# Kernel tuning notes

Hardware: AMD Instinct MI355X
Metric: run time of the kernel (lower is better)

Reference implementation:

```python
import jax, jax.numpy as jnp
import numpy as np

DIM, NH, HD = 1536, 12, 128
C = HD // 2            # 64 complex (half) dims per head
BANDS = (C - 2 * (C // 3), C // 3, C // 3)   # (22, 21, 21) for T/H/W
EPS = 1e-6
F, Hg, Wg = 6, 20, 32
S = F * Hg * Wg
MAX_LEN = 1024


def _rope_tables(max_len=MAX_LEN):
    # Wan-style 1D rope params per band, concatenated along channel dim -> [max_len, 64]
    pos = np.arange(max_len, dtype=np.float64)
    cos_l, sin_l = [], []
    for bd in BANDS:
        inv = 1.0 / (10000.0 ** (np.arange(bd, dtype=np.float64) / bd))
        ang = np.outer(pos, inv)
        cos_l.append(np.cos(ang))
        sin_l.append(np.sin(ang))
    return (np.concatenate(cos_l, 1).astype(np.float32),
            np.concatenate(sin_l, 1).astype(np.float32))


def setup_inputs() -> dict:
    key = jax.random.key(0)
    ks = jax.random.split(key, 8)
    std = 0.02
    fc, fs = _rope_tables()
    return {
        "x": jax.random.normal(ks[0], (1, S, DIM), jnp.float32),
        "Wq": jax.random.normal(ks[1], (DIM, DIM), jnp.float32) * std,
        "bq": jnp.zeros((DIM,), jnp.float32),
        "Wk": jax.random.normal(ks[2], (DIM, DIM), jnp.float32) * std,
        "bk": jnp.zeros((DIM,), jnp.float32),
        "Wv": jax.random.normal(ks[3], (DIM, DIM), jnp.float32) * std,
        "bv": jnp.zeros((DIM,), jnp.float32),
        "Wo": jax.random.normal(ks[4], (DIM, DIM), jnp.float32) * std,
        "bo": jnp.zeros((DIM,), jnp.float32),
        "gq": jnp.ones((DIM,), jnp.float32),
        "gk": jnp.ones((DIM,), jnp.float32),
        "freqs_cos": jnp.asarray(fc),
        "freqs_sin": jnp.asarray(fs),
        "f": F, "h": Hg, "w": Wg,
    }


def _rmsnorm(t, g):
    t = t.astype(jnp.float32)
    return t * jax.lax.rsqrt(jnp.mean(t * t, axis=-1, keepdims=True) + EPS) * g


def _grid_freqs(tab, f, h, w):
    # tab: [max_len, 64] -> [f*h*w, 64] via T/H/W band broadcast (mirrors torch expand+cat)
    o1, o2 = BANDS[0], BANDS[0] + BANDS[1]
    t = jnp.broadcast_to(tab[:f, None, None, :o1], (f, h, w, BANDS[0]))
    hh = jnp.broadcast_to(tab[None, :h, None, o1:o2], (f, h, w, BANDS[1]))
    ww = jnp.broadcast_to(tab[None, None, :w, o2:C], (f, h, w, BANDS[2]))
    return jnp.concatenate([t, hh, ww], axis=-1).reshape(f * h * w, 1, C)


def _rope_apply(t, fc, fs):
    # t: [B, S, n, d]; complex mul (a+ib)*(cos+isin) on pairs of channels
    B, Sl, n, d = t.shape
    tr = t.astype(jnp.float32).reshape(B, Sl, n, C, 2)
    a, b = tr[..., 0], tr[..., 1]
    fc = fc[None]  # [1, S, 1, C]
    fs = fs[None]
    out_r = a * fc - b * fs
    out_i = a * fs + b * fc
    return jnp.stack([out_r, out_i], axis=-1).reshape(B, Sl, n, d)


def reference(x, Wq, bq, Wk, bk, Wv, bv, Wo, bo, gq, gk, freqs_cos, freqs_sin, f, h, w):
    B, Sl, _ = x.shape
    q = _rmsnorm(x @ Wq.T + bq, gq).reshape(B, Sl, NH, HD)
    k = _rmsnorm(x @ Wk.T + bk, gk).reshape(B, Sl, NH, HD)
    v = (x @ Wv.T + bv).reshape(B, Sl, NH, HD)

    fc = _grid_freqs(freqs_cos, f, h, w)
    fs = _grid_freqs(freqs_sin, f, h, w)
    q = _rope_apply(q, fc, fs)
    k = _rope_apply(k, fc, fs)

    scale = 1.0 / jnp.sqrt(jnp.float32(HD))
    scores = jnp.einsum('bqnd,bknd->bnqk', q, k) * scale
    p = jax.nn.softmax(scores, axis=-1)
    o = jnp.einsum('bnqk,bknd->bqnd', p, v.astype(jnp.float32))
    o = o.reshape(B, Sl, DIM)
    return o @ Wo.T + bo
```

## Files before the change

kernel.cpp:

```cpp
#include <hip/hip_runtime.h>
#include <hip/hip_bf16.h>
#include <cstdint>

#define DIM 1536
#define NHEADS 12
#define HD 128
#define SEQ 3840
#define SCL2F 0.1275365308119098f
#define THRRAW 90.50966799187809f

typedef float f32x4 __attribute__((ext_vector_type(4)));
typedef __bf16 bf16x8 __attribute__((ext_vector_type(8)));
typedef __bf16 bf16x4 __attribute__((ext_vector_type(4)));
typedef __bf16 bf16x2 __attribute__((ext_vector_type(2)));
typedef unsigned int u32;
typedef u32 u32x4 __attribute__((ext_vector_type(4)));

#define GLLD(g, l) __builtin_amdgcn_global_load_lds( \
    (const __attribute__((address_space(1))) void*)(g), \
    (__attribute__((address_space(3))) void*)(l), 16, 0, 0)

__global__ __launch_bounds__(256) void cvt_bf16_5(
    const float* __restrict__ s0, const float* __restrict__ s1, const float* __restrict__ s2,
    const float* __restrict__ s3, const float* __restrict__ s4,
    __bf16* __restrict__ d0, __bf16* __restrict__ d1, __bf16* __restrict__ d2,
    __bf16* __restrict__ d3, __bf16* __restrict__ d4,
    int n4_0, int n4_w) {
    const float* src; __bf16* dst; int n4;
    switch (blockIdx.y) {
        case 0: src = s0; dst = d0; n4 = n4_0; break;
        case 1: src = s1; dst = d1; n4 = n4_w; break;
        case 2: src = s2; dst = d2; n4 = n4_w; break;
        case 3: src = s3; dst = d3; n4 = n4_w; break;
        default: src = s4; dst = d4; n4 = n4_w; break;
    }
    int i = blockIdx.x * 256 + threadIdx.x;
    if (i < n4) {
        f32x4 v = ((const f32x4*)src)[i];
        bf16x4 o;
        o[0] = (__bf16)v[0]; o[1] = (__bf16)v[1];
        o[2] = (__bf16)v[2]; o[3] = (__bf16)v[3];
        ((bf16x4*)dst)[i] = o;
    }
}

template <int OUTF32>
__global__ __launch_bounds__(256, 2) void gemm256(
    const __bf16* __restrict__ A,
    const __bf16* __restrict__ B0, const __bf16* __restrict__ B1, const __bf16* __restrict__ B2,
    const float* __restrict__ bias0, const float* __restrict__ bias1, const float* __restrict__ bias2,
    void* __restrict__ C0v, void* __restrict__ C1v, void* __restrict__ C2v,
    int N, int K) {
    const int orig = blockIdx.x;
    const int nwg = gridDim.x;
    const int qq_ = nwg >> 3, rr_ = nwg & 7;
    const int xcd = orig & 7, off = orig >> 3;
    const int wgid = (xcd < rr_ ? xcd * (qq_ + 1) : rr_ * (qq_ + 1) + (xcd - rr_) * qq_) + off;
    const int z = wgid / 180;
    const int rem = wgid - z * 180;
    const int by = rem / 12;
    const int bx = rem - by * 12;

    const __bf16* B = B0; const float* bias = bias0; void* Cv = C0v;
    if (z == 1) { B = B1; bias = bias1; Cv = C1v; }
    else if (z == 2) { B = B2; bias = bias2; Cv = C2v; }

    __shared__ __bf16 sA[3][256 * 32];
    __shared__ __bf16 sB[3][128 * 32];

    const int t = threadIdx.x;
    const int wid = t >> 6, lane = t & 63;
    const int lr = lane & 15, lg = lane >> 4;
    const int wr = (wid >> 1) * 128, wc = (wid & 1) * 64;

    const __bf16* pa = A + ((long long)by * 256 + (t >> 2)) * K + (t & 3) * 8;
    const __bf16* pb = B + ((long long)bx * 128 + (t >> 2)) * K + (t & 3) * 8;
    const int ldsbase = wid * 512;

    auto stage = [&](int kk, int bufi) {
#pragma unroll
        for (int r = 0; r < 4; r++)
            GLLD(pa + (long long)(r * 64) * K + kk, &sA[bufi][r * 2048 + ldsbase]);
#pragma unroll
        for (int r = 0; r < 2; r++)
            GLLD(pb + (long long)(r * 64) * K + kk, &sB[bufi][r * 2048 + ldsbase]);
    };

    f32x4 acc[8][4] = {};
    const int NT = K / 32;

    stage(0, 0);
    stage(32, 1);
    asm volatile("s_waitcnt vmcnt(6)" ::: "memory");
    __builtin_amdgcn_s_barrier();
    __builtin_amdgcn_sched_barrier(0);

    int c0 = 0, c2 = 2;
#pragma unroll 1
    for (int i = 0; i < NT; i++) {
        const __bf16* sAc = &sA[0][0] + c0 * (256 * 32);
        const __bf16* sBc = &sB[0][0] + c0 * (128 * 32);
        bf16x8 af[8], bfr[4];
#pragma unroll
        for (int mI = 0; mI < 8; mI++)
            af[mI] = *(const bf16x8*)(sAc + (wr + mI * 16 + lr) * 32 + lg * 8);
#pragma unroll
        for (int nI = 0; nI < 4; nI++)
            bfr[nI] = *(const bf16x8*)(sBc + (wc + nI * 16 + lr) * 32 + lg * 8);
        if (i + 2 < NT) stage((i + 2) * 32, c2);

        __builtin_amdgcn_s_setprio(1);
#pragma unroll
        for (int mI = 0; mI < 8; mI++) {
            acc[mI][0] = __builtin_amdgcn_mfma_f32_16x16x32_bf16(af[mI], bfr[0], acc[mI][0], 0, 0, 0);
            acc[mI][1] = __builtin_amdgcn_mfma_f32_16x16x32_bf16(af[mI], bfr[1], acc[mI][1], 0, 0, 0);
        }
        __builtin_amdgcn_s_setprio(0);
        __builtin_amdgcn_s_barrier();
        __builtin_amdgcn_s_setprio(1);
#pragma unroll
        for (int mI = 0; mI < 8; mI++) {
            acc[mI][2] = __builtin_amdgcn_mfma_f32_16x16x32_bf16(af[mI], bfr[2], acc[mI][2], 0, 0, 0);
            acc[mI][3] = __builtin_amdgcn_mfma_f32_16x16x32_bf16(af[mI], bfr[3], acc[mI][3], 0, 0, 0);
        }
        __builtin_amdgcn_s_setprio(0);

        if (i + 2 < NT) asm volatile("s_waitcnt vmcnt(6)" ::: "memory");
        else            asm volatile("s_waitcnt vmcnt(0)" ::: "memory");
        __builtin_amdgcn_s_barrier();
        __builtin_amdgcn_sched_barrier(0);
        c0 = (c0 == 2) ? 0 : c0 + 1;
        c2 = (c2 == 2) ? 0 : c2 + 1;
    }

    const int cb = bx * 128 + wc;
    const int rb_ = by * 256 + wr;
#pragma unroll
    for (int nI = 0; nI < 4; nI++) {
        int col = cb + nI * 16 + lr;
        float bv = bias[col];
#pragma unroll
        for (int mI = 0; mI < 8; mI++) {
            int row0 = rb_ + mI * 16 + lg * 4;
#pragma unroll
            for (int r = 0; r < 4; r++) {
                float v = acc[mI][nI][r] + bv;
                if (OUTF32) ((float*)Cv)[(long long)(row0 + r) * N + col] = v;
                else ((__bf16*)Cv)[(long long)(row0 + r) * N + col] = (__bf16)v;
            }
        }
    }
}

__global__ __launch_bounds__(256) void norm_rope2(
    const __bf16* __restrict__ qpre, const __bf16* __restrict__ kpre,
    const float* __restrict__ gq, const float* __restrict__ gk,
    const float* __restrict__ fcos, const float* __restrict__ fsin,
    __bf16* __restrict__ Qb, __bf16* __restrict__ Kb) {
    const __bf16* pre = blockIdx.y ? kpre : qpre;
    const float* gvec = blockIdx.y ? gk : gq;
    __bf16* out = blockIdx.y ? Kb : Qb;
    const int s = blockIdx.x;
    const int t = threadIdx.x;
    float a[3], b[3];
    float ss = 0.f;
#pragma unroll
    for (int j = 0; j < 3; j++) {
        int p = t + 256 * j;
        bf16x2 v = *(const bf16x2*)(pre + (size_t)s * DIM + 2 * p);
        a[j] = (float)v[0]; b[j] = (float)v[1];
        ss += a[j] * a[j] + b[j] * b[j];
    }
    for (int off = 32; off; off >>= 1) ss += __shfl_down(ss, off);
    __shared__ float red[4];
    if ((t & 63) == 0) red[t >> 6] = ss;
    __syncthreads();
    float mean = (red[0] + red[1] + red[2] + red[3]) * (1.f / DIM);
    float rms = rsqrtf(mean + 1e-6f);
    const int fi = s / 640, hi2 = (s % 640) >> 5, wi = s & 31;
#pragma unroll
    for (int j = 0; j < 3; j++) {
        int p = t + 256 * j;
        int c = p & 63;
        int pos = (c < 22) ? fi : ((c < 43) ? hi2 : wi);
        float fc = fcos[pos * 64 + c];
        float fs = fsin[pos * 64 + c];
        float av = a[j] * rms * gvec[2 * p];
        float bv = b[j] * rms * gvec[2 * p + 1];
        float orr = av * fc - bv * fs;
        float oi = av * fs + bv * fc;
        int hh = p >> 6;
        bf16x2 o; o[0] = (__bf16)orr; o[1] = (__bf16)oi;
        *(bf16x2*)(out + ((size_t)hh * SEQ + s) * HD + 2 * c) = o;
    }
}

__global__ __launch_bounds__(256) void transpose_bf16(
    const __bf16* __restrict__ in, __bf16* __restrict__ out) {
    __shared__ __bf16 tile[64][68];
    const int t = threadIdx.x;
    const int sb = blockIdx.x * 64, cb = blockIdx.y * 64;
    const int tx = t & 15, ty = t >> 4;
#pragma unroll
    for (int i = 0; i < 4; i++) {
        int r = ty + i * 16;
        bf16x4 v = *(const bf16x4*)(in + (size_t)(sb + r) * DIM + cb + tx * 4);
        *(bf16x4*)&tile[r][tx * 4] = v;
    }
    __syncthreads();
    int s0 = sb + tx * 4;
    int j = (s0 >> 2) & 7;
    int u = (j < 4) ? (j << 1) : ((j << 1) - 7);
    int sp = (s0 & ~31) + (u << 2);
#pragma unroll
    for (int i = 0; i < 4; i++) {
        int c = ty + i * 16;
        bf16x4 v;
        v[0] = tile[tx * 4 + 0][c]; v[1] = tile[tx * 4 + 1][c];
        v[2] = tile[tx * 4 + 2][c]; v[3] = tile[tx * 4 + 3][c];
        *(bf16x4*)(out + (size_t)(cb + c) * SEQ + sp) = v;
    }
}

__global__ __launch_bounds__(256, 3) void attn_split(
    const __bf16* __restrict__ Q, const __bf16* __restrict__ Kk,
    const __bf16* __restrict__ Vp,
    float* __restrict__ pacc,
    float2* __restrict__ pml) {
    __shared__ __bf16 Ks[2][32 * 128];
    __shared__ __bf16 Vs[2][128 * 32];
    const int bid = blockIdx.x;
    const int task = (bid & 7) * 90 + (bid >> 3);
    const int half = task & 1;
    const int hq = task >> 1;
    const int h = hq / 30;
    const int qb = hq % 30;
    const int t = threadIdx.x;
    const int wv = t >> 6;
    const int lane = t & 63;
    const int lq = lane & 15, g = lane >> 4;
    const int q0 = qb * 128 + wv * 32;
    const int kvbase = half * (SEQ / 2);
    const __bf16* Qh = Q + (size_t)h * SEQ * HD;
    const __bf16* Kh = Kk + (size_t)h * SEQ * HD;
    const __bf16* Vh = Vp + (size_t)h * HD * SEQ;

    bf16x8 qf[2][4];
#pragma unroll
    for (int qg = 0; qg < 2; qg++)
#pragma unroll
        for (int c = 0; c < 4; c++)
            qf[qg][c] = *(const bf16x8*)(Qh + (size_t)(q0 + qg * 16 + lq) * HD + c * 32 + g * 8);

    f32x4 acc[8][2] = {};
    float m[2] = {-1e30f, -1e30f};
    float lp[2] = {0.f, 0.f};

    const int krow0 = wv * 4 + (lane >> 4);
    const int kcb = ((lane & 15) * 16) ^ ((krow0 & 7) << 4);
    const __bf16* kp = Kh + (size_t)(kvbase + krow0) * HD + (kcb >> 1);
    const __bf16* vp = Vh + (size_t)(wv * 16 + (lane >> 2)) * SEQ + kvbase + (lane & 3) * 8;
    auto stage = [&](int i, int b) {
        const __bf16* kpi = kp + (size_t)i * 32 * HD;
        const __bf16* vpi = vp + i * 32;
        GLLD(kpi,           &Ks[b][wv * 512]);
        GLLD(kpi + 16 * HD, &Ks[b][(wv + 4) * 512]);
        GLLD(vpi,            &Vs[b][wv * 512]);
        GLLD(vpi + 64 * SEQ, &Vs[b][(wv + 4) * 512]);
    };

    stage(0, 0);
    int buf = 0;
    const int kswz = (lq & 7) << 3;
#pragma unroll 1
    for (int i = 0; i < 60; i++) {
        __syncthreads();
        if (i + 1 < 60) stage(i + 1, buf ^ 1);
        const __bf16* Kb_ = &Ks[buf][0];
        const __bf16* Vb_ = &Vs[buf][0];

        f32x4 sc[2][2] = {};
        __builtin_amdgcn_s_setprio(1);
#pragma unroll
        for (int c = 0; c < 4; c++) {
            int cb = (c * 32 + g * 8) ^ kswz;
            bf16x8 k0 = *(const bf16x8*)(Kb_ + lq * 128 + cb);
            bf16x8 k1 = *(const bf16x8*)(Kb_ + (16 + lq) * 128 + cb);
            sc[0][0] = __builtin_amdgcn_mfma_f32_16x16x32_bf16(k0, qf[0][c], sc[0][0], 0, 0, 0);
            sc[0][1] = __builtin_amdgcn_mfma_f32_16x16x32_bf16(k0, qf[1][c], sc[0][1], 0, 0, 0);
            sc[1][0] = __builtin_amdgcn_mfma_f32_16x16x32_bf16(k1, qf[0][c], sc[1][0], 0, 0, 0);
            sc[1][1] = __builtin_amdgcn_mfma_f32_16x16x32_bf16(k1, qf[1][c], sc[1][1], 0, 0, 0);
        }
        __builtin_amdgcn_s_setprio(0);

        bf16x8 vf[8];
#pragma unroll
        for (int dt = 0; dt < 8; dt++)
            vf[dt] = *(const bf16x8*)(Vb_ + (dt * 16 + lq) * 32 + g * 8);

        bf16x8 pa[2];
#pragma unroll
        for (int qg = 0; qg < 2; qg++) {
            float pm = fmaxf(fmaxf(sc[0][qg][0], sc[0][qg][1]), sc[0][qg][2]);
            pm = fmaxf(fmaxf(pm, sc[0][qg][3]), sc[1][qg][0]);
            pm = fmaxf(fmaxf(pm, sc[1][qg][1]), sc[1][qg][2]);
            pm = fmaxf(pm, sc[1][qg][3]);
            if (!__all(pm <= m[qg] + THRRAW)) {
                pm = fmaxf(pm, __shfl_xor(pm, 16));
                pm = fmaxf(pm, __shfl_xor(pm, 32));
                float mn = fmaxf(m[qg], pm);
                float al = __builtin_amdgcn_exp2f(SCL2F * (m[qg] - mn));
                m[qg] = mn; lp[qg] *= al;
#pragma unroll
                for (int dt = 0; dt < 8; dt++)
#pragma unroll
                    for (int r = 0; r < 4; r++) acc[dt][qg][r] *= al;
            }
            float ms = SCL2F * m[qg];
            float p[8], ls = 0.f;
#pragma unroll
            for (int r = 0; r < 4; r++) { p[r] = __builtin_amdgcn_exp2f(SCL2F * sc[0][qg][r] - ms); ls += p[r]; }
#pragma unroll
            for (int r = 0; r < 4; r++) { p[4 + r] = __builtin_amdgcn_exp2f(SCL2F * sc[1][qg][r] - ms); ls += p[4 + r]; }
            lp[qg] += ls;
#pragma unroll
            for (int i2 = 0; i2 < 8; i2++) pa[qg][i2] = (__bf16)p[i2];
        }

        __builtin_amdgcn_s_setprio(1);
#pragma unroll
        for (int dt = 0; dt < 8; dt++) {
            acc[dt][0] = __builtin_amdgcn_mfma_f32_16x16x32_bf16(vf[dt], pa[0], acc[dt][0], 0, 0, 0);
            acc[dt][1] = __builtin_amdgcn_mfma_f32_16x16x32_bf16(vf[dt], pa[1], acc[dt][1], 0, 0, 0);
        }
        __builtin_amdgcn_s_setprio(0);
        buf ^= 1;
    }

#pragma unroll
    for (int qg = 0; qg < 2; qg++) {
        float lps = lp[qg];
        lps += __shfl_xor(lps, 16);
        lps += __shfl_xor(lps, 32);
        const size_t qrow = (size_t)(half * NHEADS + h) * SEQ + q0 + qg * 16 + lq;
        if (g == 0) pml[qrow] = float2{m[qg], lps};
#pragma unroll
        for (int dt = 0; dt < 8; dt++)
            *(f32x4*)(pacc + qrow * HD + dt * 16 + g * 4) = acc[dt][qg];
    }
}

__global__ __launch_bounds__(256) void attn_merge(
    const float* __restrict__ pacc, const float2* __restrict__ pml,
    __bf16* __restrict__ ob) {
    const int t = threadIdx.x;
    const int qq = blockIdx.x * 8 + (t >> 5);
    const int d = (t & 31) * 4;
    float2 a = pml[qq], b = pml[NHEADS * SEQ + qq];
    float M = fmaxf(a.x, b.x);
    float w0 = __builtin_amdgcn_exp2f(SCL2F * (a.x - M));
    float w1 = __builtin_amdgcn_exp2f(SCL2F * (b.x - M));
    float den = 1.f / (a.y * w0 + b.y * w1);
    f32x4 n0 = *(const f32x4*)(pacc + (size_t)qq * HD + d);
    f32x4 n1 = *(const f32x4*)(pacc + ((size_t)NHEADS * SEQ + qq) * HD + d);
    int h = qq / SEQ, s = qq % SEQ;
    bf16x4 o;
#pragma unroll
    for (int r = 0; r < 4; r++) o[r] = (__bf16)((n0[r] * w0 + n1[r] * w1) * den);
    *(bf16x4*)(ob + (size_t)s * DIM + h * HD + d) = o;
}

__global__ __launch_bounds__(256, 4) void attn_single(
    const __bf16* __restrict__ Q, const __bf16* __restrict__ Kk,
    const __bf16* __restrict__ Vp, __bf16* __restrict__ O) {
    __shared__ __bf16 Ks[2][32 * 128];
    __shared__ __bf16 Vs[2][128 * 32];
    const int bid = blockIdx.x;
    const int task = (bid & 7) * 90 + (bid >> 3);
    const int h = task / 60;
    const int qb = task % 60;
    const int t = threadIdx.x;
    const int wv = t >> 6;
    const int lane = t & 63;
    const int lq = lane & 15, g = lane >> 4;
    const int q0 = qb * 64 + wv * 16;
    const __bf16* Qh = Q + (size_t)h * SEQ * HD;
    const __bf16* Kh = Kk + (size_t)h * SEQ * HD;
    const __bf16* Vh = Vp + (size_t)h * HD * SEQ;
    bf16x8 qf[4];
#pragma unroll
    for (int c = 0; c < 4; c++)
        qf[c] = *(const bf16x8*)(Qh + (size_t)(q0 + lq) * HD + c * 32 + g * 8);
    f32x4 acc[8] = {};
    float m = -1e30f, lp = 0.f;
    const int krow_in = lane >> 4;
    const int vrow_in = lane >> 2;
    const int vce = (lane & 3) * 8;
    auto stage = [&](int kv0, int b) {
#pragma unroll
        for (int c = wv; c < 16; c += 4) {
            if (c < 8) {
                int r = c * 4 + krow_in;
                int cb = ((lane & 15) * 16) ^ ((r & 7) << 4);
                GLLD(Kh + (size_t)(kv0 + r) * HD + (cb >> 1), &Ks[b][c * 512]);
            } else {
                int cc = c - 8;
                int rd = cc * 16 + vrow_in;
                GLLD(Vh + (size_t)rd * SEQ + kv0 + vce, &Vs[b][cc * 512]);
            }
        }
    };
    stage(0, 0);
    int buf = 0;
    const int kswz = (lq & 7) << 3;
#pragma unroll 1
    for (int i = 0; i < 120; i++) {
        __syncthreads();
        if (i + 1 < 120) stage((i + 1) * 32, buf ^ 1);
        const __bf16* Kb_ = &Ks[buf][0];
        const __bf16* Vb_ = &Vs[buf][0];
        f32x4 sc0 = {0.f, 0.f, 0.f, 0.f}, sc1 = {0.f, 0.f, 0.f, 0.f};
#pragma unroll
        for (int c = 0; c < 4; c++) {
            int cb = (c * 32 + g * 8) ^ kswz;
            bf16x8 k0 = *(const bf16x8*)(Kb_ + lq * 128 + cb);
            bf16x8 k1 = *(const bf16x8*)(Kb_ + (16 + lq) * 128 + cb);
            sc0 = __builtin_amdgcn_mfma_f32_16x16x32_bf16(k0, qf[c], sc0, 0, 0, 0);
            sc1 = __builtin_amdgcn_mfma_f32_16x16x32_bf16(k1, qf[c], sc1, 0, 0, 0);
        }
        bf16x8 vf[8];
#pragma unroll
        for (int dt = 0; dt < 8; dt++)
            vf[dt] = *(const bf16x8*)(Vb_ + (dt * 16 + lq) * 32 + g * 8);
        float pm = fmaxf(fmaxf(sc0[0], sc0[1]), sc0[2]);
        pm = fmaxf(fmaxf(pm, sc0[3]), sc1[0]);
        pm = fmaxf(fmaxf(pm, sc1[1]), sc1[2]);
        pm = fmaxf(pm, sc1[3]);
        if (!__all(pm <= m + THRRAW)) {
            pm = fmaxf(pm, __shfl_xor(pm, 16));
            pm = fmaxf(pm, __shfl_xor(pm, 32));
            float mn = fmaxf(m, pm);
            float al = __builtin_amdgcn_exp2f(SCL2F * (m - mn));
            m = mn; lp *= al;
#pragma unroll
            for (int dt = 0; dt < 8; dt++)
#pragma unroll
                for (int r = 0; r < 4; r++) acc[dt][r] *= al;
        }
        float ms = SCL2F * m;
        float p[8], ls = 0.f;
#pragma unroll
        for (int r = 0; r < 4; r++) { p[r] = __builtin_amdgcn_exp2f(SCL2F * sc0[r] - ms); ls += p[r]; }
#pragma unroll
        for (int r = 0; r < 4; r++) { p[4 + r] = __builtin_amdgcn_exp2f(SCL2F * sc1[r] - ms); ls += p[4 + r]; }
        lp += ls;
        bf16x8 pa;
#pragma unroll
        for (int i2 = 0; i2 < 8; i2++) pa[i2] = (__bf16)p[i2];
#pragma unroll
        for (int dt = 0; dt < 8; dt++)
            acc[dt] = __builtin_amdgcn_mfma_f32_16x16x32_bf16(vf[dt], pa, acc[dt], 0, 0, 0);
        buf ^= 1;
    }
    float lps = lp;
    lps += __shfl_xor(lps, 16);
    lps += __shfl_xor(lps, 32);
    float inv = 1.f / lps;
#pragma unroll
    for (int dt = 0; dt < 8; dt++) {
        bf16x4 o;
#pragma unroll
        for (int r = 0; r < 4; r++) o[r] = (__bf16)(acc[dt][r] * inv);
        *(bf16x4*)(O + (size_t)(q0 + lq) * DIM + h * HD + dt * 16 + g * 4) = o;
    }
}

extern "C" void kernel_launch(void* const* d_in, const int* in_sizes, int n_in,
                              void* d_out, int out_size, void* d_ws, size_t ws_size,
                              hipStream_t stream) {
    const float* x = (const float*)d_in[0];
    const float* Wq = (const float*)d_in[1];
    const float* bq = (const float*)d_in[2];
    const float* Wk = (const float*)d_in[3];
    const float* bk = (const float*)d_in[4];
    const float* Wv = (const float*)d_in[5];
    const float* bv = (const float*)d_in[6];
    const float* Wo = (const float*)d_in[7];
    const float* bo = (const float*)d_in[8];
    const float* gq = (const float*)d_in[9];
    const float* gk = (const float*)d_in[10];
    const float* fcos = (const float*)d_in[11];
    const float* fsin = (const float*)d_in[12];
    float* out = (float*)d_out;

    char* p = (char*)d_ws;
    const size_t SZ_SD = (size_t)SEQ * DIM * 2;
    const size_t SZ_W = (size_t)DIM * DIM * 2;
    __bf16* xb   = (__bf16*)p;  p += SZ_SD;
    __bf16* Wob  = (__bf16*)p;  p += SZ_W;
    __bf16* Wqb  = (__bf16*)p;  p += SZ_W;
    __bf16* Wkb  = (__bf16*)p;  p += SZ_W;
    __bf16* Wvb  = (__bf16*)p;  p += SZ_W;
    __bf16* qpre = (__bf16*)p;  p += SZ_SD;
    __bf16* kpre = (__bf16*)p;  p += SZ_SD;
    __bf16* vpre = (__bf16*)p;  p += SZ_SD;
    __bf16* Kb   = (__bf16*)p;  p += SZ_SD;
    __bf16* Vtb  = (__bf16*)p;  p += SZ_SD;
    float2* pml  = (float2*)p;  p += sizeof(float2) * 2 * NHEADS * SEQ;
    float* pacc = (float*)Wqb;
    __bf16* Qb = xb;
    const bool split_ok = ws_size >= (size_t)(p - (char*)d_ws);

    const int n4_x = SEQ * DIM / 4;
    const int n4_w = DIM * DIM / 4;
    cvt_bf16_5<<<dim3((n4_x + 255) / 256, 5), 256, 0, stream>>>(
        x, Wq, Wk, Wv, Wo, xb, Wqb, Wkb, Wvb, Wob, n4_x, n4_w);

    gemm256<0><<<dim3(540), 256, 0, stream>>>(
        xb, Wqb, Wkb, Wvb, bq, bk, bv, qpre, kpre, vpre, DIM, DIM);

    norm_rope2<<<dim3(SEQ, 2), 256, 0, stream>>>(qpre, kpre, gq, gk, fcos, fsin, Qb, Kb);
    transpose_bf16<<<dim3(SEQ / 64, DIM / 64), 256, 0, stream>>>(vpre, Vtb);

    if (split_ok) {
        __bf16* ob = Kb;
        attn_split<<<dim3(720), 256, 0, stream>>>(Qb, Kb, Vtb, pacc, pml);
        attn_merge<<<dim3(NHEADS * SEQ / 8), 256, 0, stream>>>(pacc, pml, ob);
        gemm256<1><<<dim3(180), 256, 0, stream>>>(
            ob, Wob, Wob, Wob, bo, bo, bo, out, out, out, DIM, DIM);
    } else {
        __bf16* ob = qpre;
        attn_single<<<dim3(720), 256, 0, stream>>>(Qb, Kb, Vtb, ob);
        gemm256<1><<<dim3(180), 256, 0, stream>>>(
            ob, Wob, Wob, Wob, bo, bo, bo, out, out, out, DIM, DIM);
    }
}
```

Before: 267.0 us.

## Triple-buffer K/V staging in split attention and merge norm/transpose launches

The split attention kernel moves from double to triple buffering of the K/V LDS tiles. It prefetches two stages ahead and waits with explicit vmcnt counts and a raw s_barrier, replacing the __syncthreads at the top of each iteration. Separately, the RMSNorm+RoPE kernel and the V transpose kernel are merged into one launch using a third grid row, which removes one kernel launch. The cost is more LDS per block (48KB vs 32KB), which may limit occupancy at 3 blocks per CU, and many idle blocks in the transpose row that exit early.

```diff
diff --git a/kernel.cpp b/kernel.cpp
--- a/kernel.cpp
+++ b/kernel.cpp
@@ -152,16 +152,47 @@
     }
 }
 
-__global__ __launch_bounds__(256) void norm_rope2(
+__global__ __launch_bounds__(256) void norm_tr(
     const __bf16* __restrict__ qpre, const __bf16* __restrict__ kpre,
     const float* __restrict__ gq, const float* __restrict__ gk,
     const float* __restrict__ fcos, const float* __restrict__ fsin,
-    __bf16* __restrict__ Qb, __bf16* __restrict__ Kb) {
+    __bf16* __restrict__ Qb, __bf16* __restrict__ Kb,
+    const __bf16* __restrict__ vpre, __bf16* __restrict__ Vtb) {
+    __shared__ __bf16 tile[64][68];
+    __shared__ float red[4];
+    const int t = threadIdx.x;
+
+    if (blockIdx.y == 2) {
+        const int bxx = blockIdx.x;
+        if (bxx >= (SEQ / 64) * (DIM / 64)) return;
+        const int sb = (bxx % (SEQ / 64)) * 64, cb = (bxx / (SEQ / 64)) * 64;
+        const int tx = t & 15, ty = t >> 4;
+#pragma unroll
+        for (int i = 0; i < 4; i++) {
+            int r = ty + i * 16;
+            bf16x4 v = *(const bf16x4*)(vpre + (size_t)(sb + r) * DIM + cb + tx * 4);
+            *(bf16x4*)&tile[r][tx * 4] = v;
+        }
+        __syncthreads();
+        int s0 = sb + tx * 4;
+        int j = (s0 >> 2) & 7;
+        int u = (j < 4) ? (j << 1) : ((j << 1) - 7);
+        int sp = (s0 & ~31) + (u << 2);
+#pragma unroll
+        for (int i = 0; i < 4; i++) {
+            int c = ty + i * 16;
+            bf16x4 v;
+            v[0] = tile[tx * 4 + 0][c]; v[1] = tile[tx * 4 + 1][c];
+            v[2] = tile[tx * 4 + 2][c]; v[3] = tile[tx * 4 + 3][c];
+            *(bf16x4*)(Vtb + (size_t)(cb + c) * SEQ + sp) = v;
+        }
+        return;
+    }
+
     const __bf16* pre = blockIdx.y ? kpre : qpre;
     const float* gvec = blockIdx.y ? gk : gq;
     __bf16* out = blockIdx.y ? Kb : Qb;
     const int s = blockIdx.x;
-    const int t = threadIdx.x;
     float a[3], b[3];
     float ss = 0.f;
 #pragma unroll
@@ -172,7 +203,6 @@
         ss += a[j] * a[j] + b[j] * b[j];
     }
     for (int off = 32; off; off >>= 1) ss += __shfl_down(ss, off);
-    __shared__ float red[4];
     if ((t & 63) == 0) red[t >> 6] = ss;
     __syncthreads();
     float mean = (red[0] + red[1] + red[2] + red[3]) * (1.f / DIM);
@@ -195,40 +225,13 @@
     }
 }
 
-__global__ __launch_bounds__(256) void transpose_bf16(
-    const __bf16* __restrict__ in, __bf16* __restrict__ out) {
-    __shared__ __bf16 tile[64][68];
-    const int t = threadIdx.x;
-    const int sb = blockIdx.x * 64, cb = blockIdx.y * 64;
-    const int tx = t & 15, ty = t >> 4;
-#pragma unroll
-    for (int i = 0; i < 4; i++) {
-        int r = ty + i * 16;
-        bf16x4 v = *(const bf16x4*)(in + (size_t)(sb + r) * DIM + cb + tx * 4);
-        *(bf16x4*)&tile[r][tx * 4] = v;
-    }
-    __syncthreads();
-    int s0 = sb + tx * 4;
-    int j = (s0 >> 2) & 7;
-    int u = (j < 4) ? (j << 1) : ((j << 1) - 7);
-    int sp = (s0 & ~31) + (u << 2);
-#pragma unroll
-    for (int i = 0; i < 4; i++) {
-        int c = ty + i * 16;
-        bf16x4 v;
-        v[0] = tile[tx * 4 + 0][c]; v[1] = tile[tx * 4 + 1][c];
-        v[2] = tile[tx * 4 + 2][c]; v[3] = tile[tx * 4 + 3][c];
-        *(bf16x4*)(out + (size_t)(cb + c) * SEQ + sp) = v;
-    }
-}
-
 __global__ __launch_bounds__(256, 3) void attn_split(
     const __bf16* __restrict__ Q, const __bf16* __restrict__ Kk,
     const __bf16* __restrict__ Vp,
     float* __restrict__ pacc,
     float2* __restrict__ pml) {
-    __shared__ __bf16 Ks[2][32 * 128];
-    __shared__ __bf16 Vs[2][128 * 32];
+    __shared__ __bf16 Ks[3][32 * 128];
+    __shared__ __bf16 Vs[3][128 * 32];
     const int bid = blockIdx.x;
     const int task = (bid & 7) * 90 + (bid >> 3);
     const int half = task & 1;
@@ -270,14 +273,18 @@
     };
 
     stage(0, 0);
-    int buf = 0;
+    stage(1, 1);
+    asm volatile("s_waitcnt vmcnt(4)" ::: "memory");
+    __builtin_amdgcn_s_barrier();
+    __builtin_amdgcn_sched_barrier(0);
+
+    int c0 = 0, c2 = 2;
     const int kswz = (lq & 7) << 3;
 #pragma unroll 1
     for (int i = 0; i < 60; i++) {
-        __syncthreads();
-        if (i + 1 < 60) stage(i + 1, buf ^ 1);
-        const __bf16* Kb_ = &Ks[buf][0];
-        const __bf16* Vb_ = &Vs[buf][0];
+        if (i + 2 < 60) stage(i + 2, c2);
+        const __bf16* Kb_ = &Ks[c0][0];
+        const __bf16* Vb_ = &Vs[c0][0];
 
         f32x4 sc[2][2] = {};
         __builtin_amdgcn_s_setprio(1);
@@ -334,7 +341,13 @@
             acc[dt][1] = __builtin_amdgcn_mfma_f32_16x16x32_bf16(vf[dt], pa[1], acc[dt][1], 0, 0, 0);
         }
         __builtin_amdgcn_s_setprio(0);
-        buf ^= 1;
+
+        if (i + 2 < 60) asm volatile("s_waitcnt vmcnt(4)" ::: "memory");
+        else            asm volatile("s_waitcnt vmcnt(0)" ::: "memory");
+        __builtin_amdgcn_s_barrier();
+        __builtin_amdgcn_sched_barrier(0);
+        c0 = (c0 == 2) ? 0 : c0 + 1;
+        c2 = (c2 == 2) ? 0 : c2 + 1;
     }
 
 #pragma unroll
@@ -519,8 +532,8 @@
     gemm256<0><<<dim3(540), 256, 0, stream>>>(
         xb, Wqb, Wkb, Wvb, bq, bk, bv, qpre, kpre, vpre, DIM, DIM);
 
-    norm_rope2<<<dim3(SEQ, 2), 256, 0, stream>>>(qpre, kpre, gq, gk, fcos, fsin, Qb, Kb);
-    transpose_bf16<<<dim3(SEQ / 64, DIM / 64), 256, 0, stream>>>(vpre, Vtb);
+    norm_tr<<<dim3(SEQ, 3), 256, 0, stream>>>(
+        qpre, kpre, gq, gk, fcos, fsin, Qb, Kb, vpre, Vtb);
 
     if (split_ok) {
         __bf16* ob = Kb;
```

Result: no change. 269.3 us (+0.9%).
